# Kernel tuning notes

Measured on AMD Instinct MI355X. Metric: run time of the kernel, lower is better.

## Reference

```python
import jax, jax.numpy as jnp
import numpy as np

K = 2
ALPHA = 1.0
EPS = 1e-6


def _bce_logits(x, z):
    # binary_cross_entropy_with_logits, elementwise, numerically stable
    return jax.nn.softplus(x) - x * z


def _unfold(x, i):
    # F.unfold(x, kernel_size=2i+1, padding=i) for x: [B,1,H,W] -> [B, P, H*W]
    ks = 2 * i + 1
    p = jax.lax.conv_general_dilated_patches(
        x, (ks, ks), (1, 1), [(i, i), (i, i)])  # [B, ks*ks, H, W], zero-padded
    B = x.shape[0]
    return p.reshape(B, ks * ks, -1)


def setup_inputs() -> dict:
    key = jax.random.key(0)
    k1, k2 = jax.random.split(key)
    B, H, W = 8, 512, 512
    pred = jax.random.normal(k1, (B, 1, H, W), dtype=jnp.float32)
    target = jax.random.randint(k2, (B, 1, H, W), 0, 2).astype(jnp.float32)
    return {"pred": pred, "target": target}


def reference(pred, target):
    B, _, H, W = pred.shape
    N = H * W
    bce = _bce_logits(pred, target).reshape(B, 1, N)  # [B,1,N]
    total = jnp.zeros((B, N), dtype=pred.dtype)
    for i in range(1, K + 1):
        ks = 2 * i + 1
        P = ks * ks
        c = P // 2
        up = _unfold(pred, i)                      # [B,P,N]
        ut = _unfold(target, i)                    # [B,P,N]
        vm = _unfold(jnp.ones_like(target), i) == 0  # True where padding
        cp = up[:, c:c + 1, :]                     # center logits [B,1,N]
        ct = ut[:, c:c + 1, :]
        joint = cp * up
        lab = ct * ut
        mutual = _bce_logits(joint, lab)
        pairwise = jnp.exp(-jax.nn.sigmoid(cp) * jax.nn.sigmoid(up))
        loss = bce / (mutual + ALPHA * pairwise + EPS)
        loss = jnp.where(vm, jnp.asarray(1.0, loss.dtype), loss)
        total = total + (0.5 ** (i - 1)) * (loss.sum(axis=1) / P)
    return total.mean()
```

## Files before the change

kernel.cpp:

```cpp
#include <hip/hip_runtime.h>

#define TILE 32
#define HALO 2
#define LH (TILE + HALO)
#define LW (TILE + 2 * HALO)
#define EPS 1e-6f


__device__ __forceinline__ float softplus_f(float x) {
    return fmaxf(x, 0.f) + __logf(1.f + __expf(-fabsf(x)));
}

constexpr float W_IN  = 1.0f / 9.0f + 0.02f;
constexpr float W_OUT = 0.02f;

__constant__ const int   c_dy[12] = {0, 0, 1, 1, 1, 1, 1, 2, 2, 2, 2, 2};
__constant__ const int   c_dx[12] = {1, 2, -2, -1, 0, 1, 2, -2, -1, 0, 1, 2};
__constant__ const float c_w[12]  = {W_IN, W_OUT, W_OUT, W_IN, W_IN, W_IN,
                                     W_OUT, W_OUT, W_OUT, W_OUT, W_OUT, W_OUT};

__global__ __launch_bounds__(256) void scloss_main(
    const float* __restrict__ pred, const float* __restrict__ target,
    double* __restrict__ partial, int B, int H, int W) {
    __shared__ float4 sh[LH * LW];

    const int tilesX = W / TILE;
    const int tilesPer = tilesX * (H / TILE);
    const int b = blockIdx.x / tilesPer;
    const int tile = blockIdx.x % tilesPer;
    const int ty0 = (tile / tilesX) * TILE;
    const int tx0 = (tile % tilesX) * TILE;

    const float* pbase = pred + (size_t)b * H * W;
    const float* tbase = target + (size_t)b * H * W;
    const int tid = threadIdx.x;

    for (int idx = tid; idx < LH * LW; idx += 256) {
        const int cy = idx / LW, cx = idx % LW;
        const int gy = ty0 + cy;
        const int gx = tx0 + cx - HALO;
        float p = 0.f, t = 0.f, g = -1.f, bce = 0.f;
        if (gy < H && gx >= 0 && gx < W) {
            p = pbase[gy * W + gx];
            t = tbase[gy * W + gx];
            g = __fdividef(1.f, 1.f + __expf(-p));
            bce = softplus_f(p) - p * t;
        }
        sh[idx] = make_float4(p, t, g, bce);
    }
    __syncthreads();

    const int px = tid & 31;
    const int py0 = tid >> 5;
    float acc = 0.f;

    const bool negCheck = (ty0 == 0) || (tx0 == 0) || (tx0 + TILE == W);

    constexpr int pdy[12] = {0, 0, 1, 1, 1, 1, 1, 2, 2, 2, 2, 2};
    constexpr int pdx[12] = {1, 2, -2, -1, 0, 1, 2, -2, -1, 0, 1, 2};
    constexpr float pw12[12] = {W_IN, W_OUT, W_OUT, W_IN, W_IN, W_IN,
                                W_OUT, W_OUT, W_OUT, W_OUT, W_OUT, W_OUT};

    #pragma unroll
    for (int r = 0; r < 4; ++r) {
        const int ay = py0 + r * 8;
        const float4* base = &sh[ay * LW + px + HALO];
        const float4 ca = base[0];

        {
            const float j = ca.x * ca.x;
            const float m = softplus_f(j) - j * (ca.y * ca.y);
            const float pw = __expf(-ca.z * ca.z);
            acc += __fdividef(W_IN * ca.w, m + pw + EPS);
        }

        #pragma unroll
        for (int k = 0; k < 12; ++k) {
            const float w = pw12[k];
            const float4 cb = base[pdy[k] * LW + pdx[k]];
            const float j = ca.x * cb.x;
            const float m = softplus_f(j) - j * (ca.y * cb.y);
            const float pw = __expf(-ca.z * cb.z);
            const float pv = __fdividef(w * (ca.w + cb.w), m + pw + EPS);
            acc += (cb.z < 0.f) ? w : pv;
        }

        if (negCheck) {
            const int gy = ty0 + ay, gx = tx0 + px;
            #pragma unroll
            for (int k = 0; k < 12; ++k) {
                const int ny = gy - c_dy[k], nx = gx - c_dx[k];
                if (ny < 0 || nx < 0 || nx >= W) acc += c_w[k];
            }
        }
    }

    #pragma unroll
    for (int off = 32; off > 0; off >>= 1)
        acc += __shfl_down(acc, off, 64);
    __shared__ double wsum[4];
    if ((tid & 63) == 0) wsum[tid >> 6] = (double)acc;
    __syncthreads();
    if (tid == 0)
        partial[blockIdx.x] = wsum[0] + wsum[1] + wsum[2] + wsum[3];
}

__global__ __launch_bounds__(256) void scloss_reduce(
    const double* __restrict__ partial, int n, float* __restrict__ out,
    double inv_cnt) {
    __shared__ double sm[256];
    double s = 0.0;
    for (int i = threadIdx.x; i < n; i += 256) s += partial[i];
    sm[threadIdx.x] = s;
    __syncthreads();
    for (int off = 128; off > 0; off >>= 1) {
        if (threadIdx.x < off) sm[threadIdx.x] += sm[threadIdx.x + off];
        __syncthreads();
    }
    if (threadIdx.x == 0) out[0] = (float)(sm[0] * inv_cnt);
}

extern "C" void kernel_launch(void* const* d_in, const int* in_sizes, int n_in,
                              void* d_out, int out_size, void* d_ws, size_t ws_size,
                              hipStream_t stream) {
    const float* pred   = (const float*)d_in[0];
    const float* target = (const float*)d_in[1];
    float* out = (float*)d_out;

    const int H = 512, W = 512;
    const int B = in_sizes[0] / (H * W);

    double* partial = (double*)d_ws;
    const int nblocks = B * (H / TILE) * (W / TILE);

    scloss_main<<<nblocks, 256, 0, stream>>>(pred, target, partial, B, H, W);
    scloss_reduce<<<1, 256, 0, stream>>>(partial, nblocks, out,
                                         1.0 / ((double)B * H * W));
}
```

Measured before the change: 104.1 us.

## Replace transcendentals with range-limited polynomials, pair reciprocals, fuse reduction via atomics

Replaces log1p and exp(-x) with short FMA polynomials valid on [0,1], which is where sigmoid products and exp(-|x|) lie. Reciprocals of neighbour pairs are combined into a single rcp. The separate reduction kernel is dropped in favour of a per-block float atomicAdd after a memset. Together these cut transcendental instruction pressure and one kernel launch, at the cost of approximation error and non-deterministic float summation.

```diff
diff --git a/kernel.cpp b/kernel.cpp
--- a/kernel.cpp
+++ b/kernel.cpp
@@ -7,21 +7,50 @@
 #define EPS 1e-6f
 
 
-__device__ __forceinline__ float softplus_f(float x) {
-    return fmaxf(x, 0.f) + __logf(1.f + __expf(-fabsf(x)));
-}
-
 constexpr float W_IN  = 1.0f / 9.0f + 0.02f;
 constexpr float W_OUT = 0.02f;
 
-__constant__ const int   c_dy[12] = {0, 0, 1, 1, 1, 1, 1, 2, 2, 2, 2, 2};
-__constant__ const int   c_dx[12] = {1, 2, -2, -1, 0, 1, 2, -2, -1, 0, 1, 2};
-__constant__ const float c_w[12]  = {W_IN, W_OUT, W_OUT, W_IN, W_IN, W_IN,
-                                     W_OUT, W_OUT, W_OUT, W_OUT, W_OUT, W_OUT};
+__device__ __forceinline__ float log1p_poly(float u) {
+    const float w = (u - 0.5f) * 0.6666666667f;
+    float s = 0.14285714f;
+    s = __builtin_fmaf(s, w, -0.16666667f);
+    s = __builtin_fmaf(s, w, 0.20f);
+    s = __builtin_fmaf(s, w, -0.25f);
+    s = __builtin_fmaf(s, w, 0.33333333f);
+    s = __builtin_fmaf(s, w, -0.50f);
+    s = __builtin_fmaf(s, w, 1.0f);
+    return __builtin_fmaf(s, w, 0.40546511f);
+}
+
+__device__ __forceinline__ float expneg01_poly(float x) {
+    const float z = x - 0.5f;
+    float s = -0.0083333333f;
+    s = __builtin_fmaf(s, z, 0.041666667f);
+    s = __builtin_fmaf(s, z, -0.16666667f);
+    s = __builtin_fmaf(s, z, 0.5f);
+    s = __builtin_fmaf(s, z, -1.0f);
+    s = __builtin_fmaf(s, z, 1.0f);
+    return s * 0.60653066f;
+}
+
+__device__ __forceinline__ void pair_nd(const float4 ca, const float4 cb, float w,
+                                        float& n, float& d) {
+    const float j   = ca.x * cb.x;
+    const float lab = ca.y * cb.y;
+    const float u   = __expf(-fabsf(j));
+    const float sp  = fmaxf(j, 0.f) + log1p_poly(u);
+    const float m   = sp - j * lab;
+    const float pw  = expneg01_poly(ca.z * cb.z);
+    const float dd  = m + pw + EPS;
+    const float nn  = w * (ca.w + cb.w);
+    const bool oob  = cb.z < 0.f;
+    n = oob ? w : nn;
+    d = oob ? 1.f : dd;
+}
 
 __global__ __launch_bounds__(256) void scloss_main(
     const float* __restrict__ pred, const float* __restrict__ target,
-    double* __restrict__ partial, int B, int H, int W) {
+    float* __restrict__ out, int B, int H, int W, double inv_cnt) {
     __shared__ float4 sh[LH * LW];
 
     const int tilesX = W / TILE;
@@ -43,8 +72,8 @@
         if (gy < H && gx >= 0 && gx < W) {
             p = pbase[gy * W + gx];
             t = tbase[gy * W + gx];
-            g = __fdividef(1.f, 1.f + __expf(-p));
-            bce = softplus_f(p) - p * t;
+            g = __builtin_amdgcn_rcpf(1.f + __expf(-p));
+            bce = fmaxf(p, 0.f) + log1p_poly(__expf(-fabsf(p))) - p * t;
         }
         sh[idx] = make_float4(p, t, g, bce);
     }
@@ -68,29 +97,26 @@
         const float4 ca = base[0];
 
         {
-            const float j = ca.x * ca.x;
-            const float m = softplus_f(j) - j * (ca.y * ca.y);
-            const float pw = __expf(-ca.z * ca.z);
-            acc += __fdividef(W_IN * ca.w, m + pw + EPS);
+            float n, d;
+            pair_nd(ca, ca, W_IN * 0.5f, n, d);
+            acc += n * __builtin_amdgcn_rcpf(d);
         }
 
         #pragma unroll
-        for (int k = 0; k < 12; ++k) {
-            const float w = pw12[k];
-            const float4 cb = base[pdy[k] * LW + pdx[k]];
-            const float j = ca.x * cb.x;
-            const float m = softplus_f(j) - j * (ca.y * cb.y);
-            const float pw = __expf(-ca.z * cb.z);
-            const float pv = __fdividef(w * (ca.w + cb.w), m + pw + EPS);
-            acc += (cb.z < 0.f) ? w : pv;
+        for (int k = 0; k < 12; k += 2) {
+            float n1, d1, n2, d2;
+            pair_nd(ca, base[pdy[k] * LW + pdx[k]], pw12[k], n1, d1);
+            pair_nd(ca, base[pdy[k + 1] * LW + pdx[k + 1]], pw12[k + 1], n2, d2);
+            const float num = n1 * d2 + n2 * d1;
+            acc += num * __builtin_amdgcn_rcpf(d1 * d2);
         }
 
         if (negCheck) {
             const int gy = ty0 + ay, gx = tx0 + px;
             #pragma unroll
             for (int k = 0; k < 12; ++k) {
-                const int ny = gy - c_dy[k], nx = gx - c_dx[k];
-                if (ny < 0 || nx < 0 || nx >= W) acc += c_w[k];
+                const int ny = gy - pdy[k], nx = gx - pdx[k];
+                if (ny < 0 || nx < 0 || nx >= W) acc += pw12[k];
             }
         }
     }
@@ -101,23 +127,10 @@
     __shared__ double wsum[4];
     if ((tid & 63) == 0) wsum[tid >> 6] = (double)acc;
     __syncthreads();
-    if (tid == 0)
-        partial[blockIdx.x] = wsum[0] + wsum[1] + wsum[2] + wsum[3];
-}
-
-__global__ __launch_bounds__(256) void scloss_reduce(
-    const double* __restrict__ partial, int n, float* __restrict__ out,
-    double inv_cnt) {
-    __shared__ double sm[256];
-    double s = 0.0;
-    for (int i = threadIdx.x; i < n; i += 256) s += partial[i];
-    sm[threadIdx.x] = s;
-    __syncthreads();
-    for (int off = 128; off > 0; off >>= 1) {
-        if (threadIdx.x < off) sm[threadIdx.x] += sm[threadIdx.x + off];
-        __syncthreads();
+    if (tid == 0) {
+        const double s = wsum[0] + wsum[1] + wsum[2] + wsum[3];
+        atomicAdd(out, (float)(s * inv_cnt));
     }
-    if (threadIdx.x == 0) out[0] = (float)(sm[0] * inv_cnt);
 }
 
 extern "C" void kernel_launch(void* const* d_in, const int* in_sizes, int n_in,
@@ -129,11 +142,9 @@
 
     const int H = 512, W = 512;
     const int B = in_sizes[0] / (H * W);
-
-    double* partial = (double*)d_ws;
     const int nblocks = B * (H / TILE) * (W / TILE);
 
-    scloss_main<<<nblocks, 256, 0, stream>>>(pred, target, partial, B, H, W);
-    scloss_reduce<<<1, 256, 0, stream>>>(partial, nblocks, out,
-                                         1.0 / ((double)B * H * W));
+    hipMemsetAsync(out, 0, sizeof(float), stream);
+    scloss_main<<<nblocks, 256, 0, stream>>>(pred, target, out, B, H, W,
+                                             1.0 / ((double)B * H * W));
 }
```

New measurement: 101.9 us. 2.1% less time.
